# Kernel optimization log

Measured on AMD Instinct MI355X. Metric: run time of the kernel, lower is better.

## Reference

```python
import jax, jax.numpy as jnp
import numpy as np

H = 1024
V = 50257
S = 4096
L = 2


def gru_cell(x, h, Wih, Whh, bih, bhh):
    # x: (1, in), h: (1, H); PyTorch GRUCell math
    gi = x @ Wih.T + bih  # (1, 3H)
    gh = h @ Whh.T + bhh  # (1, 3H)
    i_r, i_z, i_n = jnp.split(gi, 3, axis=1)
    h_r, h_z, h_n = jnp.split(gh, 3, axis=1)
    r = jax.nn.sigmoid(i_r + h_r)
    z = jax.nn.sigmoid(i_z + h_z)
    n = jnp.tanh(i_n + r * h_n)
    return (1.0 - z) * n + z * h


def setup_inputs() -> dict:
    key = jax.random.key(0)
    ks = jax.random.split(key, 16)
    s = 0.02
    inp = {
        "input": jax.random.randint(ks[0], (1,), 0, V),
        "last_context": jax.random.normal(ks[1], (1, H), jnp.float32),
        "hidden": jax.random.normal(ks[2], (L, 1, H), jnp.float32),
        "encoder_outputs": jax.random.normal(ks[3], (S, 1, H), jnp.float32),
        "emb": jax.random.normal(ks[4], (V, H), jnp.float32) * s,
        "attn_W": jax.random.normal(ks[5], (H, H), jnp.float32) * s,
        "attn_b": jnp.zeros((H,), jnp.float32),
        "Wih0": jax.random.normal(ks[6], (3 * H, 2 * H), jnp.float32) * s,
        "Whh0": jax.random.normal(ks[7], (3 * H, H), jnp.float32) * s,
        "bih0": jnp.zeros((3 * H,), jnp.float32),
        "bhh0": jnp.zeros((3 * H,), jnp.float32),
        "Wih1": jax.random.normal(ks[8], (3 * H, H), jnp.float32) * s,
        "Whh1": jax.random.normal(ks[9], (3 * H, H), jnp.float32) * s,
        "bih1": jnp.zeros((3 * H,), jnp.float32),
        "bhh1": jnp.zeros((3 * H,), jnp.float32),
        "out_W": jax.random.normal(ks[10], (V, 2 * H), jnp.float32) * s,
        "out_b": jnp.zeros((V,), jnp.float32),
    }
    return inp


def reference(input, last_context, hidden, encoder_outputs, emb, attn_W, attn_b,
              Wih0, Whh0, bih0, bhh0, Wih1, Whh1, bih1, bhh1, out_W, out_b):
    # Embedding lookup for the single decoded token -> (1, H)
    x = emb[input].reshape(1, H)
    rnn_in = jnp.concatenate([x, last_context], axis=1)  # (1, 2H)
    # Stacked 2-layer GRU, single timestep
    h0 = gru_cell(rnn_in, hidden[0], Wih0, Whh0, bih0, bhh0)  # (1, H)
    h1 = gru_cell(h0, hidden[1], Wih1, Whh1, bih1, bhh1)      # (1, H)
    new_hidden = jnp.stack([h0, h1], axis=0)                  # (L, 1, H)
    rnn_output = h1                                           # (1, H)
    # Additive-score attention, vectorized over all S encoder timesteps
    enc = encoder_outputs[:, 0, :]                            # (S, H)
    energies = (enc @ attn_W.T + attn_b) @ rnn_output[0]      # (S,)
    attn_w = jax.nn.softmax(energies)                         # (S,)
    context = (attn_w @ enc).reshape(1, H)                    # (1, H)
    logits = jnp.concatenate([rnn_output, context], axis=1) @ out_W.T + out_b
    output = jax.nn.log_softmax(logits, axis=-1)              # (1, V)
    return output, context, new_hidden, attn_w.reshape(1, 1, S)
```

## Files before the change

kernel.cpp:

```cpp
#include <hip/hip_runtime.h>
#include <math.h>

static constexpr int kH = 1024;
static constexpr int kV = 50257;
static constexpr int kS = 4096;
static constexpr int kLogABlocks = (kV + 3) / 4;
static constexpr int kLogBBlocks = 1024;
static constexpr float kEShift = 30.f;

__device__ __forceinline__ float wred_sum(float v) {
#pragma unroll
  for (int o = 32; o > 0; o >>= 1) v += __shfl_down(v, o, 64);
  return v;
}
__device__ __forceinline__ float wred_sum_all(float v) {
#pragma unroll
  for (int o = 32; o > 0; o >>= 1) v += __shfl_xor(v, o, 64);
  return v;
}

__global__ __launch_bounds__(256) void gru_kernel(
    const int* __restrict__ tok, const float* __restrict__ emb,
    const float* __restrict__ xa, const float* __restrict__ xb,
    const float* __restrict__ hprev,
    const float* __restrict__ Wih, const float* __restrict__ Whh,
    const float* __restrict__ bih, const float* __restrict__ bhh,
    float* __restrict__ hout, float* __restrict__ hout2,
    float* __restrict__ zu, float* __restrict__ zc, float* __restrict__ zz) {
  const int i = blockIdx.x;
  const int t = threadIdx.x;
  const int lane = t & 63, wid = t >> 6;

  if (zu) {
    if (i < 4) zu[i * 256 + t] = 0.f;
    else if (i < 8) zc[(i - 4) * 256 + t] = 0.f;
    else if (i == 8 && t == 0) zz[0] = 0.f;
  }

  const float* xrow = tok ? (emb + (size_t)tok[0] * kH) : xa;
  const int nk4 = tok ? 512 : 256;
  const size_t xw = tok ? (size_t)(2 * kH) : (size_t)kH;

  const float4* X0 = (const float4*)xrow;
  const float4* X1 = (const float4*)xb;
  const float4* Wr = (const float4*)(Wih + (size_t)i * xw);
  const float4* Wz = (const float4*)(Wih + (size_t)(kH + i) * xw);
  const float4* Wn = (const float4*)(Wih + (size_t)(2 * kH + i) * xw);
  const float4* Ur = (const float4*)(Whh + (size_t)i * kH);
  const float4* Uz = (const float4*)(Whh + (size_t)(kH + i) * kH);
  const float4* Un = (const float4*)(Whh + (size_t)(2 * kH + i) * kH);
  const float4* Hp = (const float4*)hprev;

  float ar = 0.f, az = 0.f, an = 0.f, br = 0.f, bz = 0.f, bn = 0.f;
  for (int k = t; k < nk4; k += 256) {
    const float4 x = (k < 256) ? X0[k] : X1[k - 256];
    float4 w;
    w = Wr[k]; ar += w.x * x.x + w.y * x.y + w.z * x.z + w.w * x.w;
    w = Wz[k]; az += w.x * x.x + w.y * x.y + w.z * x.z + w.w * x.w;
    w = Wn[k]; an += w.x * x.x + w.y * x.y + w.z * x.z + w.w * x.w;
  }
  {
    const float4 h = Hp[t];
    float4 w;
    w = Ur[t]; br += w.x * h.x + w.y * h.y + w.z * h.z + w.w * h.w;
    w = Uz[t]; bz += w.x * h.x + w.y * h.y + w.z * h.z + w.w * h.w;
    w = Un[t]; bn += w.x * h.x + w.y * h.y + w.z * h.z + w.w * h.w;
  }
  ar = wred_sum(ar); az = wred_sum(az); an = wred_sum(an);
  br = wred_sum(br); bz = wred_sum(bz); bn = wred_sum(bn);
  __shared__ float red[6][4];
  if (lane == 0) {
    red[0][wid] = ar; red[1][wid] = az; red[2][wid] = an;
    red[3][wid] = br; red[4][wid] = bz; red[5][wid] = bn;
  }
  __syncthreads();
  if (t == 0) {
    const float s0 = red[0][0] + red[0][1] + red[0][2] + red[0][3];
    const float s1 = red[1][0] + red[1][1] + red[1][2] + red[1][3];
    const float s2 = red[2][0] + red[2][1] + red[2][2] + red[2][3];
    const float s3 = red[3][0] + red[3][1] + red[3][2] + red[3][3];
    const float s4 = red[4][0] + red[4][1] + red[4][2] + red[4][3];
    const float s5 = red[5][0] + red[5][1] + red[5][2] + red[5][3];
    const float r = 1.f / (1.f + expf(-((s0 + bih[i]) + (s3 + bhh[i]))));
    const float z = 1.f / (1.f + expf(-((s1 + bih[kH + i]) + (s4 + bhh[kH + i]))));
    const float n = tanhf((s2 + bih[2 * kH + i]) + r * (s5 + bhh[2 * kH + i]));
    const float h = (1.f - z) * n + z * hprev[i];
    hout[i] = h;
    hout2[i] = h;
  }
}

__global__ __launch_bounds__(256) void attnu_logitsA_kernel(
    const float* __restrict__ attn_W, const float* __restrict__ h1,
    float* __restrict__ u, const float* __restrict__ out_W,
    const float* __restrict__ out_b, float* __restrict__ logits) {
  const int b = blockIdx.x;
  const int t = threadIdx.x;
  if (b < 128) {
    const int j0 = b * 8;
    const float4* W4 = (const float4*)attn_W;
    float4 acc = make_float4(0.f, 0.f, 0.f, 0.f);
#pragma unroll
    for (int j = j0; j < j0 + 8; ++j) {
      const float hj = h1[j];
      const float4 w = W4[(size_t)j * 256 + t];
      acc.x += hj * w.x; acc.y += hj * w.y;
      acc.z += hj * w.z; acc.w += hj * w.w;
    }
    atomicAdd(&u[4 * t + 0], acc.x);
    atomicAdd(&u[4 * t + 1], acc.y);
    atomicAdd(&u[4 * t + 2], acc.z);
    atomicAdd(&u[4 * t + 3], acc.w);
    return;
  }
  const int lane = t & 63;
  const int v = (b - 128) * 4 + (t >> 6);
  if (v >= kV) return;
  const float4* W = (const float4*)(out_W + (size_t)v * (2 * kH));
  const float4* X0 = (const float4*)h1;
  float acc = 0.f;
#pragma unroll
  for (int k = lane; k < 256; k += 64) {
    const float4 w = W[k];
    const float4 x = X0[k];
    acc += w.x * x.x + w.y * x.y + w.z * x.z + w.w * x.w;
  }
  acc = wred_sum(acc);
  if (lane == 0) logits[v] = acc + out_b[v];
}

__global__ __launch_bounds__(256) void attn_fused_kernel(
    const float* __restrict__ enc, const float* __restrict__ u,
    float* __restrict__ wexp, float* __restrict__ ctx, float* __restrict__ Z) {
  const int b = blockIdx.x;
  const int t = threadIdx.x;
  const int lane = t & 63, wid = t >> 6;
  __shared__ float cacc[4][kH];
  __shared__ float zred[4];

  const float4* U4 = (const float4*)u;
  float4 u4[4];
#pragma unroll
  for (int j = 0; j < 4; ++j) u4[j] = U4[lane + 64 * j];

  float4 c4[4];
#pragma unroll
  for (int j = 0; j < 4; ++j) c4[j] = make_float4(0.f, 0.f, 0.f, 0.f);
  float zp = 0.f;
  const int s0 = b * 16 + wid * 4;
#pragma unroll
  for (int r = 0; r < 4; ++r) {
    const int s = s0 + r;
    const float4* E = (const float4*)(enc + (size_t)s * kH);
    float4 e4[4];
    float acc = 0.f;
#pragma unroll
    for (int j = 0; j < 4; ++j) {
      e4[j] = E[lane + 64 * j];
      acc += e4[j].x * u4[j].x + e4[j].y * u4[j].y + e4[j].z * u4[j].z +
             e4[j].w * u4[j].w;
    }
    acc = wred_sum_all(acc);
    const float w = expf(acc - kEShift);
    if (lane == 0) { wexp[s] = w; zp += w; }
#pragma unroll
    for (int j = 0; j < 4; ++j) {
      c4[j].x += w * e4[j].x; c4[j].y += w * e4[j].y;
      c4[j].z += w * e4[j].z; c4[j].w += w * e4[j].w;
    }
  }
#pragma unroll
  for (int j = 0; j < 4; ++j)
    ((float4*)&cacc[wid][0])[lane + 64 * j] = c4[j];
  if (lane == 0) zred[wid] = zp;
  __syncthreads();
#pragma unroll
  for (int j = 0; j < 4; ++j) {
    const int idx = t + 256 * j;
    const float vsum =
        cacc[0][idx] + cacc[1][idx] + cacc[2][idx] + cacc[3][idx];
    atomicAdd(&ctx[idx], vsum);
  }
  if (t == 0) atomicAdd(Z, zred[0] + zred[1] + zred[2] + zred[3]);
}

__global__ __launch_bounds__(256) void logitsB_kernel(
    const float* __restrict__ out_W, const float* __restrict__ ctx,
    const float* __restrict__ Z, float* __restrict__ logits,
    float* __restrict__ part) {
  const int b = blockIdx.x;
  const int t = threadIdx.x;
  const int lane = t & 63, wid = t >> 6;
  __shared__ float red[2][4];

  const float invZ = 1.f / Z[0];
  const float4* X1 = (const float4*)ctx;
  float4 x1[4];
#pragma unroll
  for (int j = 0; j < 4; ++j) x1[j] = X1[lane + 64 * j];

  float lm = -INFINITY, ls = 0.f;
  for (int v = b * 4 + wid; v < kV; v += kLogBBlocks * 4) {
    const float4* W = (const float4*)(out_W + (size_t)v * (2 * kH)) + 256;
    float acc1 = 0.f;
#pragma unroll
    for (int j = 0; j < 4; ++j) {
      const float4 w = W[lane + 64 * j];
      acc1 += w.x * x1[j].x + w.y * x1[j].y + w.z * x1[j].z + w.w * x1[j].w;
    }
    const float acc = wred_sum(acc1);
    if (lane == 0) {
      const float val = logits[v] + invZ * acc;
      logits[v] = val;
      const float M2 = fmaxf(lm, val);
      ls = ls * expf(lm - M2) + expf(val - M2);
      lm = M2;
    }
  }
  if (lane == 0) { red[0][wid] = lm; red[1][wid] = ls; }
  __syncthreads();
  if (t == 0) {
    float m = red[0][0], s = red[1][0];
#pragma unroll
    for (int w = 1; w < 4; ++w) {
      const float M2 = fmaxf(m, red[0][w]);
      s = s * expf(m - M2) + red[1][w] * expf(red[0][w] - M2);
      m = M2;
    }
    part[2 * b] = m;
    part[2 * b + 1] = s;
  }
}

__global__ __launch_bounds__(256) void finalize_kernel(
    float* __restrict__ logits, const float* __restrict__ part,
    const float* __restrict__ ctx_ws, const float* __restrict__ wexp,
    const float* __restrict__ Z, float* __restrict__ o_ctx,
    float* __restrict__ o_attn) {
  const int b = blockIdx.x;
  const int t = threadIdx.x;
  const int lane = t & 63, wid = t >> 6;
  __shared__ float red[2][4];

  float m = -INFINITY, s = 0.f;
  for (int i = t; i < kLogBBlocks; i += 256) {
    const float bm = part[2 * i], bs = part[2 * i + 1];
    const float M2 = fmaxf(m, bm);
    s = s * expf(m - M2) + bs * expf(bm - M2);
    m = M2;
  }
#pragma unroll
  for (int o = 32; o > 0; o >>= 1) {
    const float m2 = __shfl_down(m, o, 64);
    const float s2 = __shfl_down(s, o, 64);
    const float M2 = fmaxf(m, m2);
    s = s * expf(m - M2) + s2 * expf(m2 - M2);
    m = M2;
  }
  if (lane == 0) { red[0][wid] = m; red[1][wid] = s; }
  __syncthreads();
  float M = red[0][0], S = red[1][0];
#pragma unroll
  for (int w = 1; w < 4; ++w) {
    const float M2 = fmaxf(M, red[0][w]);
    S = S * expf(M - M2) + red[1][w] * expf(red[0][w] - M2);
    M = M2;
  }
  const float shift = M + logf(S);
  const int v = b * 256 + t;
  if (v < kV) logits[v] -= shift;
  const float invZ = 1.f / Z[0];
  if (b < 4) o_ctx[b * 256 + t] = ctx_ws[b * 256 + t] * invZ;
  else if (b < 20) o_attn[(b - 4) * 256 + t] = wexp[(b - 4) * 256 + t] * invZ;
}

extern "C" void kernel_launch(void* const* d_in, const int* in_sizes, int n_in,
                              void* d_out, int out_size, void* d_ws,
                              size_t ws_size, hipStream_t stream) {
  const int* tok = (const int*)d_in[0];
  const float* last_ctx = (const float*)d_in[1];
  const float* hidden = (const float*)d_in[2];
  const float* enc = (const float*)d_in[3];
  const float* emb = (const float*)d_in[4];
  const float* attn_W = (const float*)d_in[5];
  const float* Wih0 = (const float*)d_in[7];
  const float* Whh0 = (const float*)d_in[8];
  const float* bih0 = (const float*)d_in[9];
  const float* bhh0 = (const float*)d_in[10];
  const float* Wih1 = (const float*)d_in[11];
  const float* Whh1 = (const float*)d_in[12];
  const float* bih1 = (const float*)d_in[13];
  const float* bhh1 = (const float*)d_in[14];
  const float* out_W = (const float*)d_in[15];
  const float* out_b = (const float*)d_in[16];

  float* out = (float*)d_out;
  float* o_logits = out;
  float* o_ctx = out + kV;
  float* o_h0 = out + kV + kH;
  float* o_h1 = out + kV + 2 * kH;
  float* o_attn = out + kV + 3 * kH;

  float* ws = (float*)d_ws;
  float* ws_u = ws;
  float* ws_h0 = ws + 1024;
  float* ws_h1 = ws + 2048;
  float* ws_ctx = ws + 3072;
  float* ws_attn = ws + 4096;
  float* ws_part = ws + 8192;
  float* ws_z = ws + 10240;

  gru_kernel<<<kH, 256, 0, stream>>>(tok, emb, nullptr, last_ctx, hidden, Wih0,
                                     Whh0, bih0, bhh0, ws_h0, o_h0, ws_u,
                                     ws_ctx, ws_z);
  gru_kernel<<<kH, 256, 0, stream>>>(nullptr, nullptr, ws_h0, nullptr,
                                     hidden + kH, Wih1, Whh1, bih1, bhh1,
                                     ws_h1, o_h1, nullptr, nullptr, nullptr);
  attnu_logitsA_kernel<<<128 + kLogABlocks, 256, 0, stream>>>(
      attn_W, ws_h1, ws_u, out_W, out_b, o_logits);
  attn_fused_kernel<<<256, 256, 0, stream>>>(enc, ws_u, ws_attn, ws_ctx,
                                             ws_z);
  logitsB_kernel<<<kLogBBlocks, 256, 0, stream>>>(out_W, ws_ctx, ws_z,
                                                  o_logits, ws_part);
  finalize_kernel<<<(kV + 255) / 256, 256, 0, stream>>>(
      o_logits, ws_part, ws_ctx, ws_attn, ws_z, o_ctx, o_attn);
}
```

Baseline: 119.7 us.

## Use persistent grid-stride logits kernels with register double-buffered weight prefetch

The first-half logits pass moves from one block per four vocab rows (about 12.5k blocks) to a fixed 2048-block grid-stride loop. Both logits kernels now prefetch the next row's weights into registers while the current row is being reduced, so loads overlap with compute. The attention kernel is split across twice as many blocks with half the rows each, and the partial-softmax buffer grows to 2048 entries with the Z slot moved to match. The aim is less block-launch overhead and more memory-level parallelism on a bandwidth-bound GEMV, at the cost of extra registers and more atomics in the attention stage.

```diff
diff --git a/kernel.cpp b/kernel.cpp
--- a/kernel.cpp
+++ b/kernel.cpp
@@ -4,8 +4,7 @@
 static constexpr int kH = 1024;
 static constexpr int kV = 50257;
 static constexpr int kS = 4096;
-static constexpr int kLogABlocks = (kV + 3) / 4;
-static constexpr int kLogBBlocks = 1024;
+static constexpr int kLogBlocks = 2048;
 static constexpr float kEShift = 30.f;
 
 __device__ __forceinline__ float wred_sum(float v) {
@@ -114,19 +113,39 @@
     return;
   }
   const int lane = t & 63;
-  const int v = (b - 128) * 4 + (t >> 6);
-  if (v >= kV) return;
-  const float4* W = (const float4*)(out_W + (size_t)v * (2 * kH));
   const float4* X0 = (const float4*)h1;
-  float acc = 0.f;
-#pragma unroll
-  for (int k = lane; k < 256; k += 64) {
-    const float4 w = W[k];
-    const float4 x = X0[k];
-    acc += w.x * x.x + w.y * x.y + w.z * x.z + w.w * x.w;
-  }
-  acc = wred_sum(acc);
-  if (lane == 0) logits[v] = acc + out_b[v];
+  float4 x0[4];
+#pragma unroll
+  for (int j = 0; j < 4; ++j) x0[j] = X0[lane + 64 * j];
+
+  const int stride = kLogBlocks * 4;
+  int v = (b - 128) * 4 + (t >> 6);
+  float4 wa[4];
+  {
+    const float4* W = (const float4*)(out_W + (size_t)v * (2 * kH));
+#pragma unroll
+    for (int j = 0; j < 4; ++j) wa[j] = W[lane + 64 * j];
+  }
+  while (true) {
+    const int vn = v + stride;
+    float4 wb[4];
+    if (vn < kV) {
+      const float4* Wn = (const float4*)(out_W + (size_t)vn * (2 * kH));
+#pragma unroll
+      for (int j = 0; j < 4; ++j) wb[j] = Wn[lane + 64 * j];
+    }
+    float acc = 0.f;
+#pragma unroll
+    for (int j = 0; j < 4; ++j)
+      acc += wa[j].x * x0[j].x + wa[j].y * x0[j].y + wa[j].z * x0[j].z +
+             wa[j].w * x0[j].w;
+    acc = wred_sum(acc);
+    if (lane == 0) logits[v] = acc + out_b[v];
+    if (vn >= kV) break;
+#pragma unroll
+    for (int j = 0; j < 4; ++j) wa[j] = wb[j];
+    v = vn;
+  }
 }
 
 __global__ __launch_bounds__(256) void attn_fused_kernel(
@@ -147,9 +166,9 @@
 #pragma unroll
   for (int j = 0; j < 4; ++j) c4[j] = make_float4(0.f, 0.f, 0.f, 0.f);
   float zp = 0.f;
-  const int s0 = b * 16 + wid * 4;
-#pragma unroll
-  for (int r = 0; r < 4; ++r) {
+  const int s0 = b * 8 + wid * 2;
+#pragma unroll
+  for (int r = 0; r < 2; ++r) {
     const int s = s0 + r;
     const float4* E = (const float4*)(enc + (size_t)s * kH);
     float4 e4[4];
@@ -199,15 +218,28 @@
 #pragma unroll
   for (int j = 0; j < 4; ++j) x1[j] = X1[lane + 64 * j];
 
+  const int stride = kLogBlocks * 4;
+  int v = b * 4 + wid;
   float lm = -INFINITY, ls = 0.f;
-  for (int v = b * 4 + wid; v < kV; v += kLogBBlocks * 4) {
+  float4 wa[4];
+  {
     const float4* W = (const float4*)(out_W + (size_t)v * (2 * kH)) + 256;
+#pragma unroll
+    for (int j = 0; j < 4; ++j) wa[j] = W[lane + 64 * j];
+  }
+  while (true) {
+    const int vn = v + stride;
+    float4 wb[4];
+    if (vn < kV) {
+      const float4* Wn = (const float4*)(out_W + (size_t)vn * (2 * kH)) + 256;
+#pragma unroll
+      for (int j = 0; j < 4; ++j) wb[j] = Wn[lane + 64 * j];
+    }
     float acc1 = 0.f;
 #pragma unroll
-    for (int j = 0; j < 4; ++j) {
-      const float4 w = W[lane + 64 * j];
-      acc1 += w.x * x1[j].x + w.y * x1[j].y + w.z * x1[j].z + w.w * x1[j].w;
-    }
+    for (int j = 0; j < 4; ++j)
+      acc1 += wa[j].x * x1[j].x + wa[j].y * x1[j].y + wa[j].z * x1[j].z +
+              wa[j].w * x1[j].w;
     const float acc = wred_sum(acc1);
     if (lane == 0) {
       const float val = logits[v] + invZ * acc;
@@ -216,6 +248,10 @@
       ls = ls * expf(lm - M2) + expf(val - M2);
       lm = M2;
     }
+    if (vn >= kV) break;
+#pragma unroll
+    for (int j = 0; j < 4; ++j) wa[j] = wb[j];
+    v = vn;
   }
   if (lane == 0) { red[0][wid] = lm; red[1][wid] = ls; }
   __syncthreads();
@@ -243,7 +279,7 @@
   __shared__ float red[2][4];
 
   float m = -INFINITY, s = 0.f;
-  for (int i = t; i < kLogBBlocks; i += 256) {
+  for (int i = t; i < kLogBlocks; i += 256) {
     const float bm = part[2 * i], bs = part[2 * i + 1];
     const float M2 = fmaxf(m, bm);
     s = s * expf(m - M2) + bs * expf(bm - M2);
@@ -308,7 +344,7 @@
   float* ws_ctx = ws + 3072;
   float* ws_attn = ws + 4096;
   float* ws_part = ws + 8192;
-  float* ws_z = ws + 10240;
+  float* ws_z = ws + 12288;
 
   gru_kernel<<<kH, 256, 0, stream>>>(tok, emb, nullptr, last_ctx, hidden, Wih0,
                                      Whh0, bih0, bhh0, ws_h0, o_h0, ws_u,
@@ -316,12 +352,12 @@
   gru_kernel<<<kH, 256, 0, stream>>>(nullptr, nullptr, ws_h0, nullptr,
                                      hidden + kH, Wih1, Whh1, bih1, bhh1,
                                      ws_h1, o_h1, nullptr, nullptr, nullptr);
-  attnu_logitsA_kernel<<<128 + kLogABlocks, 256, 0, stream>>>(
+  attnu_logitsA_kernel<<<128 + kLogBlocks, 256, 0, stream>>>(
       attn_W, ws_h1, ws_u, out_W, out_b, o_logits);
-  attn_fused_kernel<<<256, 256, 0, stream>>>(enc, ws_u, ws_attn, ws_ctx,
+  attn_fused_kernel<<<512, 256, 0, stream>>>(enc, ws_u, ws_attn, ws_ctx,
                                              ws_z);
-  logitsB_kernel<<<kLogBBlocks, 256, 0, stream>>>(out_W, ws_ctx, ws_z,
-                                                  o_logits, ws_part);
+  logitsB_kernel<<<kLogBlocks, 256, 0, stream>>>(out_W, ws_ctx, ws_z,
+                                                 o_logits, ws_part);
   finalize_kernel<<<(kV + 255) / 256, 256, 0, stream>>>(
       o_logits, ws_part, ws_ctx, ws_attn, ws_z, o_ctx, o_attn);
 }
```

Measured after the change: 134.1 us. 12.0% more time.
